# Kernel optimization log

Hardware: AMD Instinct MI355X
Metric: run time of the kernel (lower is better)

The kernel has to match this reference:

```python
import jax, jax.numpy as jnp
import numpy as np

NUM_CLASSES = 80
IMG = 608.0
L_COORD, L_NOOBJ, L_CLS = 5.0, 0.5, 1.0
EPS = 1e-7
ANCHORS = jnp.array([[12,16],[19,36],[40,28],[36,75],[76,55],[72,146],
                     [142,110],[192,243],[459,401]], dtype=jnp.float32).reshape(3, 3, 2)


def _iou(b1, b2):
    # boxes in (cx, cy, w, h); broadcastable shapes [..., 4]
    b1x1 = b1[..., 0] - b1[..., 2] * 0.5; b1y1 = b1[..., 1] - b1[..., 3] * 0.5
    b1x2 = b1[..., 0] + b1[..., 2] * 0.5; b1y2 = b1[..., 1] + b1[..., 3] * 0.5
    b2x1 = b2[..., 0] - b2[..., 2] * 0.5; b2y1 = b2[..., 1] - b2[..., 3] * 0.5
    b2x2 = b2[..., 0] + b2[..., 2] * 0.5; b2y2 = b2[..., 1] + b2[..., 3] * 0.5
    iw = jnp.clip(jnp.minimum(b1x2, b2x2) - jnp.maximum(b1x1, b2x1), 0.0)
    ih = jnp.clip(jnp.minimum(b1y2, b2y2) - jnp.maximum(b1y1, b2y1), 0.0)
    inter = iw * ih
    union = (b1x2 - b1x1) * (b1y2 - b1y1) + (b2x2 - b2x1) * (b2y2 - b2y1) - inter + EPS
    return inter / union


def _scale_loss(pred, anchors, targets):
    # pred: [B, A, H, W, 5+C]; anchors: [A, 2] (pixels); targets: [B, T, 5+C]
    B, A, H, W, _ = pred.shape
    C = pred.shape[-1] - 5
    T = targets.shape[1]

    # ---- decode predictions (decodePredictionsStable) ----
    gy, gx = jnp.meshgrid(jnp.arange(H), jnp.arange(W), indexing='ij')
    grid = jnp.stack([gx, gy], axis=-1).astype(pred.dtype)          # [H, W, 2]
    xy = jax.nn.sigmoid(pred[..., :2])
    wh = jnp.clip(pred[..., 2:4], -10.0, 10.0)
    box_xy = jnp.clip((xy + grid) / jnp.array([W, H], dtype=pred.dtype), 0.0, 1.0)
    box_wh = jnp.clip(jnp.exp(wh) * anchors[None, :, None, None, :] / IMG, 0.0, 1.0)
    pbox = jnp.concatenate([box_xy, box_wh], axis=-1)               # [B,A,H,W,4]
    pconf = jax.nn.sigmoid(pred[..., 4])                            # [B,A,H,W]
    pcls = jax.nn.sigmoid(pred[..., 5:])                            # [B,A,H,W,C]

    # ---- build targets (buildTargetsStable, vectorized scatter) ----
    gtbox = jnp.clip(targets[..., :4], 0.0, 1.0)                    # [B,T,4]
    valid = targets[..., 4] > 0                                     # [B,T]
    gxi = jnp.clip((gtbox[..., 0] * W).astype(jnp.int32), 0, W - 1)
    gyi = jnp.clip((gtbox[..., 1] * H).astype(jnp.int32), 0, H - 1)
    abox = jnp.concatenate([jnp.full((A, 2), 0.5, dtype=pred.dtype), anchors / IMG], axis=-1)
    ious = _iou(abox[None, None, :, :], gtbox[:, :, None, :])       # [B,T,A]
    best = jnp.argmax(ious, axis=-1).astype(jnp.int32)              # first max == torch strict '>' loop
    bidx = jnp.broadcast_to(jnp.arange(B, dtype=jnp.int32)[:, None], (B, T))

    flat = ((bidx * A + best) * H + gyi) * W + gxi                  # [B,T]
    order = jnp.arange(B * T, dtype=jnp.int32).reshape(B, T)
    ncells = B * A * H * W
    winner = jnp.full((ncells,), -1, jnp.int32).at[jnp.where(valid, flat, ncells)].max(order, mode='drop')
    keep = valid & (winner[flat] == order)
    bw = jnp.where(keep, bidx, B)                                   # out-of-range -> dropped

    mask = jnp.zeros((B, A, H, W), pred.dtype).at[bw, best, gyi, gxi].set(1.0, mode='drop')
    tbox = jnp.zeros((B, A, H, W, 4), pred.dtype).at[bw, best, gyi, gxi].set(gtbox, mode='drop')
    tcls = jnp.zeros((B, A, H, W, C), pred.dtype).at[bw, best, gyi, gxi].set(targets[..., 5:5 + C], mode='drop')

    npos = jnp.sum(mask)
    nneg = jnp.asarray(mask.size, pred.dtype) - npos

    # ---- coordinate loss: mean(1 - IoU) over positives ----
    coord = jnp.where(npos > 0, jnp.sum((1.0 - _iou(pbox, tbox)) * mask) / jnp.maximum(npos, 1.0), 0.0)

    # ---- confidence loss: BCE sum/npos + lambdaNoObj * BCE sum/nneg ----
    p = jnp.clip(pconf, 1e-10, 1.0 - 1e-10)
    bce = -(mask * jnp.log(p) + (1.0 - mask) * jnp.log1p(-p))
    conf = jnp.sum(bce * mask) / jnp.maximum(npos, 1.0) \
         + L_NOOBJ * jnp.sum(bce * (1.0 - mask)) / jnp.maximum(nneg, 1.0)

    # ---- class loss: BCE mean over positive rows ----
    pc = jnp.clip(pcls, 1e-10, 1.0 - 1e-10)
    tc = jnp.clip(tcls, 0.0, 1.0)
    bcec = -(tc * jnp.log(pc) + (1.0 - tc) * jnp.log1p(-pc))
    cls = jnp.where(npos > 0, jnp.sum(bcec * mask[..., None]) / jnp.maximum(npos * C, 1.0), 0.0)

    return coord, conf, cls


def setup_inputs() -> dict:
    key = jax.random.key(0)
    k0, k1, k2, k3 = jax.random.split(key, 4)
    B, T, C = 16, 50, NUM_CLASSES
    pred0 = jax.random.normal(k0, (B, 3, 76, 76, 5 + C), dtype=jnp.float32)
    pred1 = jax.random.normal(k1, (B, 3, 38, 38, 5 + C), dtype=jnp.float32)
    pred2 = jax.random.normal(k2, (B, 3, 19, 19, 5 + C), dtype=jnp.float32)
    targets = jax.random.uniform(k3, (B, T, 5 + C), dtype=jnp.float32)
    return {"pred0": pred0, "pred1": pred1, "pred2": pred2, "targets": targets}


def reference(pred0, pred1, pred2, targets):
    coord = jnp.float32(0.0); conf = jnp.float32(0.0); cls = jnp.float32(0.0)
    for s, pred in enumerate((pred0, pred1, pred2)):
        c, cf, cl = _scale_loss(pred, ANCHORS[s], targets)
        coord = coord + c; conf = conf + cf; cls = cls + cl
    total = L_COORD * coord + conf + L_CLS * cls
    return total, coord, conf, cls
```

## Files before the change

### kernel.cpp

```cpp
#include <hip/hip_runtime.h>
#include <math.h>

#define BB   16
#define TT   50
#define BT   (BB*TT)
#define NCLS 80
#define IMGF 608.0f

#define H0 76
#define H1 38
#define H2 19
#define N0 277248
#define N1 69312
#define N2 17328
#define NTOT (N0+N1+N2)

#define CELLS_PER_THREAD 8
#define NOOBJ_BLOCKS ((NTOT + 256*CELLS_PER_THREAD - 1) / (256*CELLS_PER_THREAD))

#define POS_BLOCKS_PER_SCALE 200
#define NPOS_BLOCKS (3*POS_BLOCKS_PER_SCALE)
#define NBLK (NOOBJ_BLOCKS + NPOS_BLOCKS)

__constant__ float c_anchors[3][3][2] = {
    {{12.f,16.f},{19.f,36.f},{40.f,28.f}},
    {{36.f,75.f},{76.f,55.f},{72.f,146.f}},
    {{142.f,110.f},{192.f,243.f},{459.f,401.f}}};
__constant__ int c_H[3] = {H0, H1, H2};

__device__ __forceinline__ float sigmoidf_(float x) { return 1.0f / (1.0f + expf(-x)); }
__device__ __forceinline__ float clipf_(float x, float lo, float hi) {
    return fminf(fmaxf(x, lo), hi);
}

__device__ __forceinline__ float iou4(float ax, float ay, float aw, float ah,
                                      float bx, float by, float bw, float bh) {
    float ax1 = ax - aw * 0.5f, ay1 = ay - ah * 0.5f;
    float ax2 = ax + aw * 0.5f, ay2 = ay + ah * 0.5f;
    float bx1 = bx - bw * 0.5f, by1 = by - bh * 0.5f;
    float bx2 = bx + bw * 0.5f, by2 = by + bh * 0.5f;
    float iw = fmaxf(fminf(ax2, bx2) - fmaxf(ax1, bx1), 0.f);
    float ih = fmaxf(fminf(ay2, by2) - fmaxf(ay1, by1), 0.f);
    float inter = iw * ih;
    float uni = (ax2 - ax1) * (ay2 - ay1) + (bx2 - bx1) * (by2 - by1) - inter + 1e-7f;
    return inter / uni;
}

__device__ __forceinline__ int target_cell(const float* tr, int s, float& cx, float& cy,
                                           float& w, float& h, int& best, int& gxi, int& gyi) {
    float t4 = tr[4];
    if (!(t4 > 0.f)) return -1;
    cx = clipf_(tr[0], 0.f, 1.f);
    cy = clipf_(tr[1], 0.f, 1.f);
    w  = clipf_(tr[2], 0.f, 1.f);
    h  = clipf_(tr[3], 0.f, 1.f);
    best = 0;
    float bi = -1e30f;
    #pragma unroll
    for (int a = 0; a < 3; a++) {
        float aw = c_anchors[s][a][0] / IMGF;
        float ah = c_anchors[s][a][1] / IMGF;
        float v = iou4(0.5f, 0.5f, aw, ah, cx, cy, w, h);
        if (v > bi) { bi = v; best = a; }
    }
    int H = c_H[s];
    gxi = (int)(cx * (float)H); gxi = min(max(gxi, 0), H - 1);
    gyi = (int)(cy * (float)H); gyi = min(max(gyi, 0), H - 1);
    return 0;
}

__global__ __launch_bounds__(256) void k_main(const float* __restrict__ p0,
                                              const float* __restrict__ p1,
                                              const float* __restrict__ p2,
                                              const float* __restrict__ targets,
                                              float* __restrict__ noobj_part,
                                              float* __restrict__ pos_part) {
    int blk = blockIdx.x;
    int lane = threadIdx.x & 63;
    int wv = threadIdx.x >> 6;

    if (blk < NOOBJ_BLOCKS) {
        int base = blk * (256 * CELLS_PER_THREAD) + threadIdx.x;
        float vals[CELLS_PER_THREAD];
        #pragma unroll
        for (int k = 0; k < CELLS_PER_THREAD; k++) {
            int g = base + k * 256;
            const float* pred; int c;
            if (g < N0)            { pred = p0; c = g; }
            else if (g < N0 + N1)  { pred = p1; c = g - N0; }
            else                   { pred = p2; c = g - N0 - N1; }
            vals[k] = (g < NTOT) ? pred[(long long)c * 85 + 4] : 0.f;
        }
        float sum[3] = {0.f, 0.f, 0.f};
        #pragma unroll
        for (int k = 0; k < CELLS_PER_THREAD; k++) {
            int g = base + k * 256;
            if (g < NTOT) {
                float p = clipf_(sigmoidf_(vals[k]), 1e-10f, 1.0f);
                float v = -log1pf(-p);
                if (g < N0)           sum[0] += v;
                else if (g < N0 + N1) sum[1] += v;
                else                  sum[2] += v;
            }
        }
        #pragma unroll
        for (int off = 32; off > 0; off >>= 1) {
            sum[0] += __shfl_xor(sum[0], off, 64);
            sum[1] += __shfl_xor(sum[1], off, 64);
            sum[2] += __shfl_xor(sum[2], off, 64);
        }
        __shared__ float sm[4][3];
        if (lane == 0) { sm[wv][0] = sum[0]; sm[wv][1] = sum[1]; sm[wv][2] = sum[2]; }
        __syncthreads();
        if (threadIdx.x < 3)
            noobj_part[blk * 3 + threadIdx.x] =
                sm[0][threadIdx.x] + sm[1][threadIdx.x] + sm[2][threadIdx.x] + sm[3][threadIdx.x];
    } else {
        int bp = blk - NOOBJ_BLOCKS;
        int s = bp / POS_BLOCKS_PER_SCALE;
        int order = (bp % POS_BLOCKS_PER_SCALE) * 4 + wv;

        float v_coord = 0.f, v_obj = 0.f, v_noadj = 0.f, v_cls = 0.f, v_np = 0.f;

        int b = order / TT, t = order % TT;
        const float* tr = targets + order * 85;
        float cx, cy, w, h; int best, gxi, gyi;
        if (target_cell(tr, s, cx, cy, w, h, best, gxi, gyi) == 0) {
            int H = c_H[s];
            int flat = ((b * 3 + best) * H + gyi) * H + gxi;

            bool lost = false;
            int tp = t + 1 + lane;
            if (tp < TT) {
                const float* tr2 = targets + (b * TT + tp) * 85;
                float cx2, cy2, w2, h2; int best2, gxi2, gyi2;
                if (target_cell(tr2, s, cx2, cy2, w2, h2, best2, gxi2, gyi2) == 0) {
                    int flat2 = ((b * 3 + best2) * H + gyi2) * H + gxi2;
                    lost = (flat2 == flat);
                }
            }
            if (__ballot(lost) == 0ull) {
                const float* pred = (s == 0) ? p0 : (s == 1) ? p1 : p2;
                const float* pc = pred + (long long)flat * 85;

                float px = sigmoidf_(pc[0]);
                float py = sigmoidf_(pc[1]);
                float bx = clipf_((px + (float)gxi) / (float)H, 0.f, 1.f);
                float by = clipf_((py + (float)gyi) / (float)H, 0.f, 1.f);
                float aw = c_anchors[s][best][0], ah = c_anchors[s][best][1];
                float bwv = clipf_(expf(clipf_(pc[2], -10.f, 10.f)) * aw / IMGF, 0.f, 1.f);
                float bhv = clipf_(expf(clipf_(pc[3], -10.f, 10.f)) * ah / IMGF, 0.f, 1.f);
                float iou = iou4(bx, by, bwv, bhv, cx, cy, w, h);

                float p = clipf_(sigmoidf_(pc[4]), 1e-10f, 1.0f);

                float pcv = clipf_(sigmoidf_(pc[5 + lane]), 1e-10f, 1.0f);
                float tc  = clipf_(tr[5 + lane], 0.f, 1.f);
                float cl  = -(tc * logf(pcv) + (1.f - tc) * log1pf(-pcv));
                if (lane < NCLS - 64) {
                    float pcv2 = clipf_(sigmoidf_(pc[5 + 64 + lane]), 1e-10f, 1.0f);
                    float tc2  = clipf_(tr[5 + 64 + lane], 0.f, 1.f);
                    cl += -(tc2 * logf(pcv2) + (1.f - tc2) * log1pf(-pcv2));
                }
                #pragma unroll
                for (int off = 32; off > 0; off >>= 1) cl += __shfl_xor(cl, off, 64);

                v_coord = 1.f - iou;
                v_obj   = -logf(p);
                v_noadj = -log1pf(-p);
                v_cls   = cl;
                v_np    = 1.f;
            }
        }

        __shared__ float psum[4][5];
        if (lane == 0) {
            psum[wv][0] = v_coord; psum[wv][1] = v_obj; psum[wv][2] = v_noadj;
            psum[wv][3] = v_cls;   psum[wv][4] = v_np;
        }
        __syncthreads();
        if (threadIdx.x < 5) {
            pos_part[bp * 5 + threadIdx.x] =
                psum[0][threadIdx.x] + psum[1][threadIdx.x] +
                psum[2][threadIdx.x] + psum[3][threadIdx.x];
        }
    }
}

__global__ __launch_bounds__(256) void k_final(const float* __restrict__ noobj_part,
                                               const float* __restrict__ pos_part,
                                               float* __restrict__ out) {
    float nsum[3] = {0.f, 0.f, 0.f};
    for (int i = threadIdx.x; i < NOOBJ_BLOCKS; i += 256) {
        #pragma unroll
        for (int s = 0; s < 3; s++) nsum[s] += noobj_part[i * 3 + s];
    }
    float ps[3][5] = {};
    for (int i = threadIdx.x; i < NPOS_BLOCKS; i += 256) {
        int s = i / POS_BLOCKS_PER_SCALE;
        #pragma unroll
        for (int q = 0; q < 5; q++) ps[s][q] += pos_part[i * 5 + q];
    }

    __shared__ float red[18][256];
    #pragma unroll
    for (int s = 0; s < 3; s++) {
        red[s][threadIdx.x] = nsum[s];
        #pragma unroll
        for (int q = 0; q < 5; q++) red[3 + s * 5 + q][threadIdx.x] = ps[s][q];
    }
    __syncthreads();
    for (int off = 128; off > 0; off >>= 1) {
        if (threadIdx.x < off) {
            #pragma unroll
            for (int r = 0; r < 18; r++)
                red[r][threadIdx.x] += red[r][threadIdx.x + off];
        }
        __syncthreads();
    }
    if (threadIdx.x == 0) {
        const float ncell[3] = {(float)N0, (float)N1, (float)N2};
        float coord = 0.f, conf = 0.f, cls = 0.f;
        #pragma unroll
        for (int s = 0; s < 3; s++) {
            float noobjTot = red[s][0];
            float co    = red[3 + s * 5 + 0][0];
            float ob    = red[3 + s * 5 + 1][0];
            float noadj = red[3 + s * 5 + 2][0];
            float cl    = red[3 + s * 5 + 3][0];
            float npos  = red[3 + s * 5 + 4][0];
            float nneg = ncell[s] - npos;
            float dn = fmaxf(npos, 1.f);
            conf += ob / dn + 0.5f * (noobjTot - noadj) / fmaxf(nneg, 1.f);
            if (npos > 0.f) {
                coord += co / dn;
                cls   += cl / fmaxf(npos * (float)NCLS, 1.f);
            }
        }
        out[0] = 5.0f * coord + conf + 1.0f * cls;
        out[1] = coord;
        out[2] = conf;
        out[3] = cls;
    }
}

extern "C" void kernel_launch(void* const* d_in, const int* in_sizes, int n_in,
                              void* d_out, int out_size, void* d_ws, size_t ws_size,
                              hipStream_t stream) {
    const float* p0 = (const float*)d_in[0];
    const float* p1 = (const float*)d_in[1];
    const float* p2 = (const float*)d_in[2];
    const float* tg = (const float*)d_in[3];
    float* out = (float*)d_out;

    char* ws = (char*)d_ws;
    float* noobj_part = (float*)ws;
    float* pos_part   = (float*)(ws + 4096);

    k_main<<<NBLK, 256, 0, stream>>>(p0, p1, p2, tg, noobj_part, pos_part);
    k_final<<<1, 256, 0, stream>>>(noobj_part, pos_part, out);
}
```

Before: 160.4 us.

## Fuse final reduction into main kernel via cooperative grid sync

Merges the two kernels into one cooperative launch: all blocks write partial sums, a grid-wide sync follows, and block 0 does the final reduction with wave shuffles instead of a shared-memory tree. The no-object term is rewritten as a softplus with a clamp in place of sigmoid followed by log1p. This removes the second kernel launch and its dependency gap. In exchange every block pays for a grid barrier, and the launch needs all NBLK blocks (about 778) to be co-resident, which the launch-bounds hint of 4 blocks per CU is meant to allow.

Result: slower. 235.1 us (+46.6%).

```diff
diff --git a/kernel.cpp b/kernel.cpp
--- a/kernel.cpp
+++ b/kernel.cpp
@@ -1,5 +1,8 @@
 #include <hip/hip_runtime.h>
+#include <hip/hip_cooperative_groups.h>
 #include <math.h>
+
+namespace cg = cooperative_groups;
 
 #define BB   16
 #define TT   50
@@ -69,15 +72,20 @@
     return 0;
 }
 
-__global__ __launch_bounds__(256) void k_main(const float* __restrict__ p0,
-                                              const float* __restrict__ p1,
-                                              const float* __restrict__ p2,
-                                              const float* __restrict__ targets,
-                                              float* __restrict__ noobj_part,
-                                              float* __restrict__ pos_part) {
+__global__ __launch_bounds__(256, 4) void k_all(const float* __restrict__ p0,
+                                                const float* __restrict__ p1,
+                                                const float* __restrict__ p2,
+                                                const float* __restrict__ targets,
+                                                float* __restrict__ noobj_part,
+                                                float* __restrict__ pos_part,
+                                                float* __restrict__ out) {
     int blk = blockIdx.x;
     int lane = threadIdx.x & 63;
     int wv = threadIdx.x >> 6;
+
+    __shared__ float sm3[4][3];
+    __shared__ float sm5[4][5];
+    __shared__ float fin[4][18];
 
     if (blk < NOOBJ_BLOCKS) {
         int base = blk * (256 * CELLS_PER_THREAD) + threadIdx.x;
@@ -96,8 +104,9 @@
         for (int k = 0; k < CELLS_PER_THREAD; k++) {
             int g = base + k * 256;
             if (g < NTOT) {
-                float p = clipf_(sigmoidf_(vals[k]), 1e-10f, 1.0f);
-                float v = -log1pf(-p);
+                float x = vals[k];
+                float sp = fmaxf(x, 0.f) + log1pf(expf(-fabsf(x)));
+                float v = fminf(sp, 23.02585093f);
                 if (g < N0)           sum[0] += v;
                 else if (g < N0 + N1) sum[1] += v;
                 else                  sum[2] += v;
@@ -109,12 +118,11 @@
             sum[1] += __shfl_xor(sum[1], off, 64);
             sum[2] += __shfl_xor(sum[2], off, 64);
         }
-        __shared__ float sm[4][3];
-        if (lane == 0) { sm[wv][0] = sum[0]; sm[wv][1] = sum[1]; sm[wv][2] = sum[2]; }
+        if (lane == 0) { sm3[wv][0] = sum[0]; sm3[wv][1] = sum[1]; sm3[wv][2] = sum[2]; }
         __syncthreads();
         if (threadIdx.x < 3)
             noobj_part[blk * 3 + threadIdx.x] =
-                sm[0][threadIdx.x] + sm[1][threadIdx.x] + sm[2][threadIdx.x] + sm[3][threadIdx.x];
+                sm3[0][threadIdx.x] + sm3[1][threadIdx.x] + sm3[2][threadIdx.x] + sm3[3][threadIdx.x];
     } else {
         int bp = blk - NOOBJ_BLOCKS;
         int s = bp / POS_BLOCKS_PER_SCALE;
@@ -173,74 +181,80 @@
             }
         }
 
-        __shared__ float psum[4][5];
         if (lane == 0) {
-            psum[wv][0] = v_coord; psum[wv][1] = v_obj; psum[wv][2] = v_noadj;
-            psum[wv][3] = v_cls;   psum[wv][4] = v_np;
+            sm5[wv][0] = v_coord; sm5[wv][1] = v_obj; sm5[wv][2] = v_noadj;
+            sm5[wv][3] = v_cls;   sm5[wv][4] = v_np;
         }
         __syncthreads();
         if (threadIdx.x < 5) {
             pos_part[bp * 5 + threadIdx.x] =
-                psum[0][threadIdx.x] + psum[1][threadIdx.x] +
-                psum[2][threadIdx.x] + psum[3][threadIdx.x];
+                sm5[0][threadIdx.x] + sm5[1][threadIdx.x] +
+                sm5[2][threadIdx.x] + sm5[3][threadIdx.x];
         }
     }
-}
-
-__global__ __launch_bounds__(256) void k_final(const float* __restrict__ noobj_part,
-                                               const float* __restrict__ pos_part,
-                                               float* __restrict__ out) {
-    float nsum[3] = {0.f, 0.f, 0.f};
-    for (int i = threadIdx.x; i < NOOBJ_BLOCKS; i += 256) {
-        #pragma unroll
-        for (int s = 0; s < 3; s++) nsum[s] += noobj_part[i * 3 + s];
-    }
-    float ps[3][5] = {};
-    for (int i = threadIdx.x; i < NPOS_BLOCKS; i += 256) {
-        int s = i / POS_BLOCKS_PER_SCALE;
-        #pragma unroll
-        for (int q = 0; q < 5; q++) ps[s][q] += pos_part[i * 5 + q];
-    }
-
-    __shared__ float red[18][256];
-    #pragma unroll
-    for (int s = 0; s < 3; s++) {
-        red[s][threadIdx.x] = nsum[s];
-        #pragma unroll
-        for (int q = 0; q < 5; q++) red[3 + s * 5 + q][threadIdx.x] = ps[s][q];
-    }
-    __syncthreads();
-    for (int off = 128; off > 0; off >>= 1) {
-        if (threadIdx.x < off) {
+
+    cg::this_grid().sync();
+
+    if (blk == 0) {
+        float acc[18];
+        #pragma unroll
+        for (int r = 0; r < 18; r++) acc[r] = 0.f;
+
+        if (threadIdx.x < NOOBJ_BLOCKS) {
+            acc[0] = noobj_part[threadIdx.x * 3 + 0];
+            acc[1] = noobj_part[threadIdx.x * 3 + 1];
+            acc[2] = noobj_part[threadIdx.x * 3 + 2];
+        }
+        #pragma unroll
+        for (int r = 0; r < 3; r++) {
+            int i = threadIdx.x + r * 256;
+            if (i < NPOS_BLOCKS) {
+                float v0 = pos_part[i * 5 + 0];
+                float v1 = pos_part[i * 5 + 1];
+                float v2 = pos_part[i * 5 + 2];
+                float v3 = pos_part[i * 5 + 3];
+                float v4 = pos_part[i * 5 + 4];
+                int s = i / POS_BLOCKS_PER_SCALE;
+                if (s == 0)      { acc[3]  += v0; acc[4]  += v1; acc[5]  += v2; acc[6]  += v3; acc[7]  += v4; }
+                else if (s == 1) { acc[8]  += v0; acc[9]  += v1; acc[10] += v2; acc[11] += v3; acc[12] += v4; }
+                else             { acc[13] += v0; acc[14] += v1; acc[15] += v2; acc[16] += v3; acc[17] += v4; }
+            }
+        }
+
+        #pragma unroll
+        for (int off = 32; off > 0; off >>= 1) {
             #pragma unroll
-            for (int r = 0; r < 18; r++)
-                red[r][threadIdx.x] += red[r][threadIdx.x + off];
+            for (int r = 0; r < 18; r++) acc[r] += __shfl_xor(acc[r], off, 64);
+        }
+        if (lane == 0) {
+            #pragma unroll
+            for (int r = 0; r < 18; r++) fin[wv][r] = acc[r];
         }
         __syncthreads();
-    }
-    if (threadIdx.x == 0) {
-        const float ncell[3] = {(float)N0, (float)N1, (float)N2};
-        float coord = 0.f, conf = 0.f, cls = 0.f;
-        #pragma unroll
-        for (int s = 0; s < 3; s++) {
-            float noobjTot = red[s][0];
-            float co    = red[3 + s * 5 + 0][0];
-            float ob    = red[3 + s * 5 + 1][0];
-            float noadj = red[3 + s * 5 + 2][0];
-            float cl    = red[3 + s * 5 + 3][0];
-            float npos  = red[3 + s * 5 + 4][0];
-            float nneg = ncell[s] - npos;
-            float dn = fmaxf(npos, 1.f);
-            conf += ob / dn + 0.5f * (noobjTot - noadj) / fmaxf(nneg, 1.f);
-            if (npos > 0.f) {
-                coord += co / dn;
-                cls   += cl / fmaxf(npos * (float)NCLS, 1.f);
-            }
-        }
-        out[0] = 5.0f * coord + conf + 1.0f * cls;
-        out[1] = coord;
-        out[2] = conf;
-        out[3] = cls;
+        if (threadIdx.x == 0) {
+            const float ncell[3] = {(float)N0, (float)N1, (float)N2};
+            float coord = 0.f, conf = 0.f, cls = 0.f;
+            #pragma unroll
+            for (int s = 0; s < 3; s++) {
+                float noobjTot = fin[0][s] + fin[1][s] + fin[2][s] + fin[3][s];
+                float co    = fin[0][3 + s * 5 + 0] + fin[1][3 + s * 5 + 0] + fin[2][3 + s * 5 + 0] + fin[3][3 + s * 5 + 0];
+                float ob    = fin[0][3 + s * 5 + 1] + fin[1][3 + s * 5 + 1] + fin[2][3 + s * 5 + 1] + fin[3][3 + s * 5 + 1];
+                float noadj = fin[0][3 + s * 5 + 2] + fin[1][3 + s * 5 + 2] + fin[2][3 + s * 5 + 2] + fin[3][3 + s * 5 + 2];
+                float cl    = fin[0][3 + s * 5 + 3] + fin[1][3 + s * 5 + 3] + fin[2][3 + s * 5 + 3] + fin[3][3 + s * 5 + 3];
+                float npos  = fin[0][3 + s * 5 + 4] + fin[1][3 + s * 5 + 4] + fin[2][3 + s * 5 + 4] + fin[3][3 + s * 5 + 4];
+                float nneg = ncell[s] - npos;
+                float dn = fmaxf(npos, 1.f);
+                conf += ob / dn + 0.5f * (noobjTot - noadj) / fmaxf(nneg, 1.f);
+                if (npos > 0.f) {
+                    coord += co / dn;
+                    cls   += cl / fmaxf(npos * (float)NCLS, 1.f);
+                }
+            }
+            out[0] = 5.0f * coord + conf + 1.0f * cls;
+            out[1] = coord;
+            out[2] = conf;
+            out[3] = cls;
+        }
     }
 }
 
@@ -257,6 +271,7 @@
     float* noobj_part = (float*)ws;
     float* pos_part   = (float*)(ws + 4096);
 
-    k_main<<<NBLK, 256, 0, stream>>>(p0, p1, p2, tg, noobj_part, pos_part);
-    k_final<<<1, 256, 0, stream>>>(noobj_part, pos_part, out);
-}
+    void* kargs[] = {(void*)&p0, (void*)&p1, (void*)&p2, (void*)&tg,
+                     (void*)&noobj_part, (void*)&pos_part, (void*)&out};
+    hipLaunchCooperativeKernel((const void*)k_all, dim3(NBLK), dim3(256), kargs, 0, stream);
+}
```

## Stream prediction tensors with coalesced float4 loads for the no-object term

Applied to the files above, without the earlier changes.

Replaces the strided per-cell load of the objectness logit with a fully coalesced float4 sweep over all prediction tensors, selecting the element at channel 4 via modular index arithmetic. The intent is to remove the cost of uncoalesced 340-byte-strided accesses, at the expense of reading every byte of the tensors instead of one element per cell. The BCE is also rewritten as a numerically stable softplus with an equivalent clamp. Block counts and the workspace layout are resized to match.

Result: slower. 177.9 us (+10.9%).

```diff
diff --git a/kernel.cpp b/kernel.cpp
--- a/kernel.cpp
+++ b/kernel.cpp
@@ -3,7 +3,6 @@
 
 #define BB   16
 #define TT   50
-#define BT   (BB*TT)
 #define NCLS 80
 #define IMGF 608.0f
 
@@ -15,12 +14,17 @@
 #define N2 17328
 #define NTOT (N0+N1+N2)
 
-#define CELLS_PER_THREAD 8
-#define NOOBJ_BLOCKS ((NTOT + 256*CELLS_PER_THREAD - 1) / (256*CELLS_PER_THREAD))
+#define C0 5891520
+#define C1 1472880
+#define C2 368220
+#define FTOT (C0+C1+C2)
 
 #define POS_BLOCKS_PER_SCALE 200
 #define NPOS_BLOCKS (3*POS_BLOCKS_PER_SCALE)
-#define NBLK (NOOBJ_BLOCKS + NPOS_BLOCKS)
+
+#define NOB 1024
+#define F4_PER_THREAD 30
+#define NBLK (NPOS_BLOCKS + NOB)
 
 __constant__ float c_anchors[3][3][2] = {
     {{12.f,16.f},{19.f,36.f},{40.f,28.f}},
@@ -79,44 +83,63 @@
     int lane = threadIdx.x & 63;
     int wv = threadIdx.x >> 6;
 
-    if (blk < NOOBJ_BLOCKS) {
-        int base = blk * (256 * CELLS_PER_THREAD) + threadIdx.x;
-        float vals[CELLS_PER_THREAD];
-        #pragma unroll
-        for (int k = 0; k < CELLS_PER_THREAD; k++) {
-            int g = base + k * 256;
-            const float* pred; int c;
-            if (g < N0)            { pred = p0; c = g; }
-            else if (g < N0 + N1)  { pred = p1; c = g - N0; }
-            else                   { pred = p2; c = g - N0 - N1; }
-            vals[k] = (g < NTOT) ? pred[(long long)c * 85 + 4] : 0.f;
-        }
-        float sum[3] = {0.f, 0.f, 0.f};
-        #pragma unroll
-        for (int k = 0; k < CELLS_PER_THREAD; k++) {
-            int g = base + k * 256;
-            if (g < NTOT) {
-                float p = clipf_(sigmoidf_(vals[k]), 1e-10f, 1.0f);
-                float v = -log1pf(-p);
-                if (g < N0)           sum[0] += v;
-                else if (g < N0 + N1) sum[1] += v;
-                else                  sum[2] += v;
+    __shared__ float sm3[4][3];
+    __shared__ float sm5[4][5];
+
+    if (blk >= NPOS_BLOCKS) {
+        int nb = blk - NPOS_BLOCKS;
+        int gbase = nb * (F4_PER_THREAD * 256) + threadIdx.x;
+        const float4* pv0 = (const float4*)p0;
+        const float4* pv1 = (const float4*)p1;
+        const float4* pv2 = (const float4*)p2;
+
+        float s0 = 0.f, s1 = 0.f, s2 = 0.f;
+        #pragma unroll 1
+        for (int c = 0; c < 6; c++) {
+            float4 v[5];
+            #pragma unroll
+            for (int j = 0; j < 5; j++) {
+                int g = gbase + (c * 5 + j) * 256;
+                const float4* pp; int q;
+                if (g < C0)            { pp = pv0; q = g; }
+                else if (g < C0 + C1)  { pp = pv1; q = g - C0; }
+                else                   { pp = pv2; q = g - (C0 + C1); }
+                v[j] = (g < FTOT) ? pp[q] : make_float4(0.f, 0.f, 0.f, 0.f);
+            }
+            #pragma unroll
+            for (int j = 0; j < 5; j++) {
+                int g = gbase + (c * 5 + j) * 256;
+                if (g < FTOT) {
+                    unsigned q = (g < C0) ? (unsigned)g
+                               : (g < C0 + C1) ? (unsigned)(g - C0)
+                               : (unsigned)(g - (C0 + C1));
+                    unsigned m = (4u * q) % 85u;
+                    if (m - 1u <= 3u) {
+                        float4 vv = v[j];
+                        float x = (m == 4u) ? vv.x : (m == 3u) ? vv.y
+                                : (m == 2u) ? vv.z : vv.w;
+                        float sp = fmaxf(x, 0.f) + log1pf(expf(-fabsf(x)));
+                        float bce = fminf(sp, 23.02585093f);
+                        if (g < C0)           s0 += bce;
+                        else if (g < C0 + C1) s1 += bce;
+                        else                  s2 += bce;
+                    }
+                }
             }
         }
         #pragma unroll
         for (int off = 32; off > 0; off >>= 1) {
-            sum[0] += __shfl_xor(sum[0], off, 64);
-            sum[1] += __shfl_xor(sum[1], off, 64);
-            sum[2] += __shfl_xor(sum[2], off, 64);
-        }
-        __shared__ float sm[4][3];
-        if (lane == 0) { sm[wv][0] = sum[0]; sm[wv][1] = sum[1]; sm[wv][2] = sum[2]; }
+            s0 += __shfl_xor(s0, off, 64);
+            s1 += __shfl_xor(s1, off, 64);
+            s2 += __shfl_xor(s2, off, 64);
+        }
+        if (lane == 0) { sm3[wv][0] = s0; sm3[wv][1] = s1; sm3[wv][2] = s2; }
         __syncthreads();
         if (threadIdx.x < 3)
-            noobj_part[blk * 3 + threadIdx.x] =
-                sm[0][threadIdx.x] + sm[1][threadIdx.x] + sm[2][threadIdx.x] + sm[3][threadIdx.x];
+            noobj_part[nb * 3 + threadIdx.x] =
+                sm3[0][threadIdx.x] + sm3[1][threadIdx.x] + sm3[2][threadIdx.x] + sm3[3][threadIdx.x];
     } else {
-        int bp = blk - NOOBJ_BLOCKS;
+        int bp = blk;
         int s = bp / POS_BLOCKS_PER_SCALE;
         int order = (bp % POS_BLOCKS_PER_SCALE) * 4 + wv;
 
@@ -173,16 +196,15 @@
             }
         }
 
-        __shared__ float psum[4][5];
         if (lane == 0) {
-            psum[wv][0] = v_coord; psum[wv][1] = v_obj; psum[wv][2] = v_noadj;
-            psum[wv][3] = v_cls;   psum[wv][4] = v_np;
+            sm5[wv][0] = v_coord; sm5[wv][1] = v_obj; sm5[wv][2] = v_noadj;
+            sm5[wv][3] = v_cls;   sm5[wv][4] = v_np;
         }
         __syncthreads();
         if (threadIdx.x < 5) {
             pos_part[bp * 5 + threadIdx.x] =
-                psum[0][threadIdx.x] + psum[1][threadIdx.x] +
-                psum[2][threadIdx.x] + psum[3][threadIdx.x];
+                sm5[0][threadIdx.x] + sm5[1][threadIdx.x] +
+                sm5[2][threadIdx.x] + sm5[3][threadIdx.x];
         }
     }
 }
@@ -191,9 +213,12 @@
                                                const float* __restrict__ pos_part,
                                                float* __restrict__ out) {
     float nsum[3] = {0.f, 0.f, 0.f};
-    for (int i = threadIdx.x; i < NOOBJ_BLOCKS; i += 256) {
-        #pragma unroll
-        for (int s = 0; s < 3; s++) nsum[s] += noobj_part[i * 3 + s];
+    #pragma unroll
+    for (int r = 0; r < 4; r++) {
+        int i = threadIdx.x + r * 256;
+        nsum[0] += noobj_part[i * 3 + 0];
+        nsum[1] += noobj_part[i * 3 + 1];
+        nsum[2] += noobj_part[i * 3 + 2];
     }
     float ps[3][5] = {};
     for (int i = threadIdx.x; i < NPOS_BLOCKS; i += 256) {
@@ -255,7 +280,7 @@
 
     char* ws = (char*)d_ws;
     float* noobj_part = (float*)ws;
-    float* pos_part   = (float*)(ws + 4096);
+    float* pos_part   = (float*)(ws + 16384);
 
     k_main<<<NBLK, 256, 0, stream>>>(p0, p1, p2, tg, noobj_part, pos_part);
     k_final<<<1, 256, 0, stream>>>(noobj_part, pos_part, out);
```
